# Optimization experiments

Hardware: AMD Instinct MI355X
Metric: run time of the kernel (lower is better)

## Reference

```python
import jax, jax.numpy as jnp
import numpy as np

B, S, D, H = 4, 2048, 1024, 16
HD = D // H  # head_dim = 64

def setup_inputs() -> dict:
    key = jax.random.key(0)
    ks = jax.random.split(key, 5)
    scale = 1.0 / np.sqrt(D)
    return {
        "x": jax.random.normal(ks[0], (B, S, D), dtype=jnp.float32),
        "Wqkv": jax.random.normal(ks[1], (D, 3 * D), dtype=jnp.float32) * scale,
        "bqkv": jax.random.normal(ks[2], (3 * D,), dtype=jnp.float32) * 0.01,
        "Wo": jax.random.normal(ks[3], (D, D), dtype=jnp.float32) * scale,
        "bo": jax.random.normal(ks[4], (D,), dtype=jnp.float32) * 0.01,
    }

def reference(x, Wqkv, bqkv, Wo, bo):
    b, s, d = x.shape
    # fused QKV projection: [B,S,3D]
    qkv = jnp.einsum("bsd,de->bse", x, Wqkv) + bqkv
    # [B,S,H,3*HD] -> [B,H,S,3*HD], then chunk into q,k,v per head
    qkv = qkv.reshape(b, s, H, 3 * HD).transpose(0, 2, 1, 3)
    q, k, v = jnp.split(qkv, 3, axis=-1)  # each [B,H,S,HD]
    inv_sqrt_dk = jnp.asarray(1.0 / np.sqrt(HD), dtype=x.dtype)
    scores = jnp.einsum("bhqd,bhkd->bhqk", q, k) * inv_sqrt_dk
    attn = jax.nn.softmax(scores, axis=-1)
    values = jnp.einsum("bhqk,bhkd->bhqd", attn, v)  # [B,H,S,HD]
    # NOTE: source reshapes [B,H,S,HD] -> [B,S,H*HD] WITHOUT permuting back
    # (a quirk of the original code); replicated faithfully.
    values = values.reshape(b, s, d)
    out = jnp.einsum("bsd,de->bse", values, Wo) + bo
    return out
```

## Files before the change

### kernel.cpp

```cpp
#include <hip/hip_runtime.h>
#include <hip/hip_bf16.h>
#include <cstdint>

static constexpr int Bq  = 4;
static constexpr int Sq  = 2048;
static constexpr int Dq  = 1024;
static constexpr int Hq  = 16;
static constexpr int HDq = 64;
static constexpr int ROWS = Bq * Sq;
static constexpr int QKV_N = 3 * Dq;

typedef __bf16 bf16x8 __attribute__((ext_vector_type(8)));
typedef __bf16 bf16x4 __attribute__((ext_vector_type(4)));
typedef __bf16 bf16x2 __attribute__((ext_vector_type(2)));
typedef float  floatx4 __attribute__((ext_vector_type(4)));
typedef float  floatx16 __attribute__((ext_vector_type(16)));
typedef unsigned int uintx4 __attribute__((ext_vector_type(4)));

#define MFMA16(a, b, c) __builtin_amdgcn_mfma_f32_16x16x32_bf16((a), (b), (c), 0, 0, 0)
#define MFMA32(a, b, c) __builtin_amdgcn_mfma_f32_32x32x16_bf16((a), (b), (c), 0, 0, 0)

#define QSCALE 0.18033688011112042f

__device__ __forceinline__ void async16(const void* g, void* l) {
    __builtin_amdgcn_global_load_lds(
        (const __attribute__((address_space(1))) uint32_t*)g,
        (__attribute__((address_space(3))) uint32_t*)l, 16, 0, 0);
}

__global__ __launch_bounds__(256) void prep_kernel(const float4* __restrict__ x4,
                                                   bf16x4* __restrict__ xb4,
                                                   const float* __restrict__ Wqkv,
                                                   __bf16* __restrict__ WqkvT,
                                                   const float* __restrict__ Wo,
                                                   __bf16* __restrict__ WoT) {
    __shared__ float t[32][33];
    const int bx = blockIdx.x;
    if (bx < 8192) {
        int i = bx * 256 + threadIdx.x;
        float4 v = x4[i];
        bf16x4 o;
        o[0] = (__bf16)v.x; o[1] = (__bf16)v.y; o[2] = (__bf16)v.z; o[3] = (__bf16)v.w;
        xb4[i] = o;
        return;
    }
    const float* in; __bf16* out; int K, N, bid;
    if (bx < 8192 + 3072) { bid = bx - 8192;  in = Wqkv; out = WqkvT; K = Dq; N = QKV_N; }
    else                  { bid = bx - 11264; in = Wo;   out = WoT;   K = Dq; N = Dq; }
    const int nt = N / 32;
    const int n0 = (bid % nt) * 32, k0 = (bid / nt) * 32;
    const int c = threadIdx.x & 31, r0 = threadIdx.x >> 5;
#pragma unroll
    for (int rr = 0; rr < 32; rr += 8)
        t[r0 + rr][c] = in[(size_t)(k0 + r0 + rr) * N + n0 + c];
    __syncthreads();
#pragma unroll
    for (int rr = 0; rr < 32; rr += 8)
        out[(size_t)(n0 + r0 + rr) * K + k0 + c] = (__bf16)t[c][r0 + rr];
}

__global__ __launch_bounds__(512, 2) void gemm_qkv_kernel(const __bf16* __restrict__ A,
                                                          const __bf16* __restrict__ BT,
                                                          const float* __restrict__ bias,
                                                          __bf16* __restrict__ qkvb,
                                                          __bf16* __restrict__ Vt) {
    __shared__ __bf16 lds[2][7][64][64];

    const int tid  = threadIdx.x;
    const int lane = tid & 63;
    const int wave = tid >> 6;
    const int wm = wave >> 1;
    const int wn = wave & 1;
    const int l31 = lane & 31;
    const int hi  = lane >> 5;
    const int kx  = l31 & 7;

    const int m0 = blockIdx.y * 256;
    const int n0 = blockIdx.x * 192;

    const int sw = ((lane & 7) ^ (lane >> 3)) * 8;
    const __bf16* gA = A  + (size_t)(m0 + wave * 8 + (lane >> 3)) * 1024 + sw;
    const __bf16* gB = BT + (size_t)(n0 + wave * 8 + (lane >> 3)) * 1024 + sw;

    auto STAGEA = [&](int buf, int u, int ktel) {
        async16(gA + (size_t)u * 65536 + ktel, &lds[buf][u][0][0] + wave * 512 + lane * 8);
    };
    auto STAGEB = [&](int buf, int j, int ktel) {
        async16(gB + (size_t)j * 65536 + ktel, &lds[buf][4 + j][0][0] + wave * 512 + lane * 8);
    };

    floatx16 acc[2][3] = {};

#pragma unroll
    for (int u = 0; u < 4; ++u) STAGEA(0, u, 0);
#pragma unroll
    for (int j = 0; j < 3; ++j) STAGEB(0, j, 0);
#pragma unroll
    for (int u = 0; u < 4; ++u) STAGEA(1, u, 64);
    asm volatile("s_waitcnt vmcnt(4)" ::: "memory");
    __builtin_amdgcn_sched_barrier(0);
    __builtin_amdgcn_s_barrier();

    bf16x8 af[2][4], bf[4];

    for (int t = 0; t < 16; ++t) {
        const int d = t & 1;

#pragma unroll
        for (int fm = 0; fm < 2; ++fm)
#pragma unroll
            for (int ks = 0; ks < 4; ++ks)
                af[fm][ks] = *(const bf16x8*)(&lds[d][wm][fm * 32 + l31][((ks * 2 + hi) ^ kx) * 8]);
        {
            const int br = wn * 96;
#pragma unroll
            for (int ks = 0; ks < 4; ++ks)
                bf[ks] = *(const bf16x8*)(&lds[d][4 + (br >> 6)][(br & 63) + l31][((ks * 2 + hi) ^ kx) * 8]);
        }
        if (t + 1 < 16) {
            STAGEB(d ^ 1, 0, (t + 1) * 64);
            STAGEB(d ^ 1, 1, (t + 1) * 64);
            STAGEB(d ^ 1, 2, (t + 1) * 64);
        }
        __builtin_amdgcn_s_barrier();
        __builtin_amdgcn_s_setprio(1);
#pragma unroll
        for (int ks = 0; ks < 4; ++ks) {
            acc[0][0] = MFMA32(af[0][ks], bf[ks], acc[0][0]);
            acc[1][0] = MFMA32(af[1][ks], bf[ks], acc[1][0]);
        }
        __builtin_amdgcn_s_setprio(0);
        __builtin_amdgcn_s_barrier();

        {
            const int br = wn * 96 + 32;
#pragma unroll
            for (int ks = 0; ks < 4; ++ks)
                bf[ks] = *(const bf16x8*)(&lds[d][4 + (br >> 6)][(br & 63) + l31][((ks * 2 + hi) ^ kx) * 8]);
        }
        if (t + 2 < 16) {
            STAGEA(d, 0, (t + 2) * 64);
            STAGEA(d, 1, (t + 2) * 64);
        }
        __builtin_amdgcn_s_barrier();
        __builtin_amdgcn_s_setprio(1);
#pragma unroll
        for (int ks = 0; ks < 4; ++ks) {
            acc[0][1] = MFMA32(af[0][ks], bf[ks], acc[0][1]);
            acc[1][1] = MFMA32(af[1][ks], bf[ks], acc[1][1]);
        }
        __builtin_amdgcn_s_setprio(0);
        __builtin_amdgcn_s_barrier();

        {
            const int br = wn * 96 + 64;
#pragma unroll
            for (int ks = 0; ks < 4; ++ks)
                bf[ks] = *(const bf16x8*)(&lds[d][4 + (br >> 6)][(br & 63) + l31][((ks * 2 + hi) ^ kx) * 8]);
        }
        if (t + 2 < 16) {
            STAGEA(d, 2, (t + 2) * 64);
            STAGEA(d, 3, (t + 2) * 64);
        }
        __builtin_amdgcn_s_barrier();
        __builtin_amdgcn_s_setprio(1);
#pragma unroll
        for (int ks = 0; ks < 4; ++ks) {
            acc[0][2] = MFMA32(af[0][ks], bf[ks], acc[0][2]);
            acc[1][2] = MFMA32(af[1][ks], bf[ks], acc[1][2]);
        }
        __builtin_amdgcn_s_setprio(0);
        if (t < 14) {
            asm volatile("s_waitcnt vmcnt(4)" ::: "memory");
        } else {
            asm volatile("s_waitcnt vmcnt(0)" ::: "memory");
        }
        __builtin_amdgcn_sched_barrier(0);
        __builtin_amdgcn_s_barrier();
    }

#pragma unroll
    for (int fn = 0; fn < 3; ++fn) {
        const int cm = wn * 96 + fn * 32;
        const int cg = n0 + cm;
        const float bv = bias[cg + l31];
        if (cm >= 128) {
            const int hh = n0 / 192;
            const int dd = cm - 128 + l31;
            const int bb = m0 >> 11;
            const int sb = (m0 & 2047) + wm * 64;
            __bf16* vt = Vt + ((size_t)(bb * Hq + hh) * HDq + dd) * Sq + sb;
#pragma unroll
            for (int fm = 0; fm < 2; ++fm)
#pragma unroll
                for (int g = 0; g < 4; ++g) {
                    bf16x4 vv;
#pragma unroll
                    for (int i = 0; i < 4; ++i) vv[i] = (__bf16)(acc[fm][fn][g * 4 + i] + bv);
                    *(bf16x4*)(vt + fm * 32 + g * 8 + hi * 4) = vv;
                }
        } else {
            const float sc = (cm < 64) ? QSCALE : 1.0f;
#pragma unroll
            for (int fm = 0; fm < 2; ++fm)
#pragma unroll
                for (int r = 0; r < 16; ++r) {
                    int m = m0 + wm * 64 + fm * 32 + (r & 3) + 8 * (r >> 2) + 4 * hi;
                    qkvb[(size_t)m * QKV_N + cg + l31] = (__bf16)((acc[fm][fn][r] + bv) * sc);
                }
        }
    }
}

__global__ __launch_bounds__(512, 2) void gemm_out_kernel(const __bf16* __restrict__ A,
                                                          const __bf16* __restrict__ BT,
                                                          const float* __restrict__ bias,
                                                          float* __restrict__ Cout) {
    __shared__ __bf16 lds[2][6][64][64];

    const int tid  = threadIdx.x;
    const int lane = tid & 63;
    const int wave = tid >> 6;
    const int wm = wave >> 1;
    const int wn = wave & 1;
    const int l31 = lane & 31;
    const int hi  = lane >> 5;
    const int kx  = l31 & 7;

    const int m0 = blockIdx.y * 256;
    const int n0 = blockIdx.x * 128;

    const int sw = ((lane & 7) ^ (lane >> 3)) * 8;
    const __bf16* gA = A  + (size_t)(m0 + wave * 8 + (lane >> 3)) * 1024 + sw;
    const __bf16* gB = BT + (size_t)(n0 + wave * 8 + (lane >> 3)) * 1024 + sw;

    auto STAGEA = [&](int buf, int u, int ktel) {
        async16(gA + (size_t)u * 65536 + ktel, &lds[buf][u][0][0] + wave * 512 + lane * 8);
    };
    auto STAGEB = [&](int buf, int j, int ktel) {
        async16(gB + (size_t)j * 65536 + ktel, &lds[buf][4 + j][0][0] + wave * 512 + lane * 8);
    };

    floatx16 acc[2][2] = {};

#pragma unroll
    for (int u = 0; u < 4; ++u) STAGEA(0, u, 0);
#pragma unroll
    for (int j = 0; j < 2; ++j) STAGEB(0, j, 0);
#pragma unroll
    for (int u = 0; u < 4; ++u) STAGEA(1, u, 64);
    asm volatile("s_waitcnt vmcnt(4)" ::: "memory");
    __builtin_amdgcn_sched_barrier(0);
    __builtin_amdgcn_s_barrier();

    bf16x8 af[2][4], bf[4];

    for (int t = 0; t < 16; ++t) {
        const int d = t & 1;

#pragma unroll
        for (int fm = 0; fm < 2; ++fm)
#pragma unroll
            for (int ks = 0; ks < 4; ++ks)
                af[fm][ks] = *(const bf16x8*)(&lds[d][wm][fm * 32 + l31][((ks * 2 + hi) ^ kx) * 8]);
#pragma unroll
        for (int ks = 0; ks < 4; ++ks)
            bf[ks] = *(const bf16x8*)(&lds[d][4 + wn][l31][((ks * 2 + hi) ^ kx) * 8]);
        if (t + 1 < 16) {
            STAGEB(d ^ 1, 0, (t + 1) * 64);
            STAGEB(d ^ 1, 1, (t + 1) * 64);
        }
        __builtin_amdgcn_s_barrier();
        __builtin_amdgcn_s_setprio(1);
#pragma unroll
        for (int ks = 0; ks < 4; ++ks) {
            acc[0][0] = MFMA32(af[0][ks], bf[ks], acc[0][0]);
            acc[1][0] = MFMA32(af[1][ks], bf[ks], acc[1][0]);
        }
        __builtin_amdgcn_s_setprio(0);
        __builtin_amdgcn_s_barrier();

#pragma unroll
        for (int ks = 0; ks < 4; ++ks)
            bf[ks] = *(const bf16x8*)(&lds[d][4 + wn][32 + l31][((ks * 2 + hi) ^ kx) * 8]);
        if (t + 2 < 16) {
            STAGEA(d, 0, (t + 2) * 64);
            STAGEA(d, 1, (t + 2) * 64);
            STAGEA(d, 2, (t + 2) * 64);
            STAGEA(d, 3, (t + 2) * 64);
        }
        __builtin_amdgcn_s_barrier();
        __builtin_amdgcn_s_setprio(1);
#pragma unroll
        for (int ks = 0; ks < 4; ++ks) {
            acc[0][1] = MFMA32(af[0][ks], bf[ks], acc[0][1]);
            acc[1][1] = MFMA32(af[1][ks], bf[ks], acc[1][1]);
        }
        __builtin_amdgcn_s_setprio(0);
        if (t < 14) {
            asm volatile("s_waitcnt vmcnt(4)" ::: "memory");
        } else {
            asm volatile("s_waitcnt vmcnt(0)" ::: "memory");
        }
        __builtin_amdgcn_sched_barrier(0);
        __builtin_amdgcn_s_barrier();
    }

#pragma unroll
    for (int fn = 0; fn < 2; ++fn) {
        const int col = n0 + wn * 64 + fn * 32 + l31;
        const float bv = bias[col];
#pragma unroll
        for (int fm = 0; fm < 2; ++fm)
#pragma unroll
            for (int r = 0; r < 16; ++r) {
                int row = m0 + wm * 64 + fm * 32 + (r & 3) + 8 * (r >> 2) + 4 * hi;
                Cout[(size_t)row * Dq + col] = acc[fm][fn][r] + bv;
            }
    }
}

__global__ __launch_bounds__(256, 2) void attn_kernel(const __bf16* __restrict__ qkv,
                                                      const __bf16* __restrict__ Vt,
                                                      __bf16* __restrict__ v2) {
    const int bh = blockIdx.x;
    const int b = bh >> 4, h = bh & 15;
    const int q0 = blockIdx.y * 256;
    const int tid  = threadIdx.x;
    const int lane = tid & 63;
    const int wave = tid >> 6;
    const int l31  = lane & 31;
    const int hi   = lane >> 5;
    const int kx   = l31 & 7;
    const size_t rs = QKV_N;
    const __bf16* base  = qkv + (size_t)b * Sq * rs + (size_t)h * (3 * HDq);
    const __bf16* vbase = Vt + (size_t)bh * HDq * Sq;

    __shared__ alignas(16) __bf16 Ks[2][64][64];
    __shared__ alignas(16) __bf16 Vs[2][64][64];

    bf16x8 qb[2][4];
#pragma unroll
    for (int qg = 0; qg < 2; ++qg) {
        const __bf16* qr = base + (size_t)(q0 + wave * 64 + qg * 32 + l31) * rs + hi * 8;
#pragma unroll
        for (int st = 0; st < 4; ++st) qb[qg][st] = *(const bf16x8*)(qr + st * 16);
    }

    const int rA = wave * 8 + (lane >> 3);
    const int rB = rA + 32;
    const int sw = ((lane & 7) ^ (rA & 7)) * 8;
    const __bf16* gK0 = base + HDq + (size_t)rA * rs + sw;
    const __bf16* gK1 = base + HDq + (size_t)rB * rs + sw;
    const __bf16* gV0 = vbase + (size_t)rA * Sq + sw;
    const __bf16* gV1 = vbase + (size_t)rB * Sq + sw;
    const int loff0 = wave * 512 + lane * 8;
    const int loff1 = (4 + wave) * 512 + lane * 8;

    auto STAGE = [&](int bufi, int kt) {
        const size_t ko = (size_t)kt * rs;
        async16(gK0 + ko, &Ks[bufi][0][0] + loff0);
        async16(gK1 + ko, &Ks[bufi][0][0] + loff1);
        async16(gV0 + kt, &Vs[bufi][0][0] + loff0);
        async16(gV1 + kt, &Vs[bufi][0][0] + loff1);
    };

    auto softmax_pb = [&](const floatx16& c, float& la, bf16x8* pb) {
        unsigned int W[8];
        float s0 = 0.f, s1 = 0.f;
#pragma unroll
        for (int m = 0; m < 8; ++m) {
            float e0 = __builtin_amdgcn_exp2f(c[2 * m]);
            float e1 = __builtin_amdgcn_exp2f(c[2 * m + 1]);
            s0 += e0; s1 += e1;
            union { bf16x2 v; unsigned int u; } pk;
            pk.v[0] = (__bf16)e0; pk.v[1] = (__bf16)e1;
            W[m] = pk.u;
        }
        la += s0 + s1;
#pragma unroll
        for (int ks = 0; ks < 2; ++ks) {
            auto r0 = __builtin_amdgcn_permlane32_swap(W[ks * 4 + 0], W[ks * 4 + 2], false, false);
            auto r1 = __builtin_amdgcn_permlane32_swap(W[ks * 4 + 1], W[ks * 4 + 3], false, false);
            uintx4 bb; bb[0] = r0[0]; bb[1] = r1[0]; bb[2] = r0[1]; bb[3] = r1[1];
            pb[ks] = __builtin_bit_cast(bf16x8, bb);
        }
    };

    floatx16 o[2][2] = {};
    float la0 = 0.f, la1 = 0.f;

    STAGE(0, 0);
    __syncthreads();

    int cur = 0;
    for (int kt = 0; kt < Sq; kt += 64, cur ^= 1) {
        if (kt + 64 < Sq) STAGE(cur ^ 1, kt + 64);

        bf16x8 ka0[4], ka1[4];
#pragma unroll
        for (int st = 0; st < 4; ++st) {
            ka0[st] = *(const bf16x8*)(&Ks[cur][l31][((st * 2 + hi) ^ kx) * 8]);
            ka1[st] = *(const bf16x8*)(&Ks[cur][32 + l31][((st * 2 + hi) ^ kx) * 8]);
        }
        floatx16 c00 = {}, c01 = {}, c10 = {}, c11 = {};
        __builtin_amdgcn_s_setprio(1);
#pragma unroll
        for (int st = 0; st < 4; ++st) {
            c00 = MFMA32(ka0[st], qb[0][st], c00);
            c10 = MFMA32(ka1[st], qb[0][st], c10);
            c01 = MFMA32(ka0[st], qb[1][st], c01);
            c11 = MFMA32(ka1[st], qb[1][st], c11);
        }
        __builtin_amdgcn_s_setprio(0);

        bf16x8 pb00[2], pb01[2], pb10[2], pb11[2];
        softmax_pb(c00, la0, pb00);
        softmax_pb(c01, la1, pb01);
        __builtin_amdgcn_s_setprio(1);
#pragma unroll
        for (int ks = 0; ks < 2; ++ks) {
            const int kslot = ks * 2 + hi;
            bf16x8 va0 = *(const bf16x8*)(&Vs[cur][l31][(kslot ^ kx) * 8]);
            bf16x8 va1 = *(const bf16x8*)(&Vs[cur][32 + l31][(kslot ^ kx) * 8]);
            o[0][0] = MFMA32(va0, pb00[ks], o[0][0]);
            o[0][1] = MFMA32(va1, pb00[ks], o[0][1]);
            o[1][0] = MFMA32(va0, pb01[ks], o[1][0]);
            o[1][1] = MFMA32(va1, pb01[ks], o[1][1]);
        }
        __builtin_amdgcn_s_setprio(0);
        softmax_pb(c10, la0, pb10);
        softmax_pb(c11, la1, pb11);
        __builtin_amdgcn_s_setprio(1);
#pragma unroll
        for (int ks = 0; ks < 2; ++ks) {
            const int kslot = 4 + ks * 2 + hi;
            bf16x8 va0 = *(const bf16x8*)(&Vs[cur][l31][(kslot ^ kx) * 8]);
            bf16x8 va1 = *(const bf16x8*)(&Vs[cur][32 + l31][(kslot ^ kx) * 8]);
            o[0][0] = MFMA32(va0, pb10[ks], o[0][0]);
            o[0][1] = MFMA32(va1, pb10[ks], o[0][1]);
            o[1][0] = MFMA32(va0, pb11[ks], o[1][0]);
            o[1][1] = MFMA32(va1, pb11[ks], o[1][1]);
        }
        __builtin_amdgcn_s_setprio(0);

        __syncthreads();
    }

#pragma unroll
    for (int qg = 0; qg < 2; ++qg) {
        float lsum = qg ? la1 : la0;
        float l = lsum + __shfl_xor(lsum, 32);
        float rinv = 1.0f / l;
        const int q = q0 + wave * 64 + qg * 32 + l31;
        size_t row = (size_t)b * Sq + h * 128 + (q >> 4);
        __bf16* vrow = v2 + row * Dq + (size_t)(q & 15) * 64;
#pragma unroll
        for (int gg = 0; gg < 4; ++gg) {
            bf16x4 ov;
#pragma unroll
            for (int i = 0; i < 4; ++i) ov[i] = (__bf16)(o[qg][0][gg * 4 + i] * rinv);
            *(bf16x4*)(vrow + gg * 8 + hi * 4) = ov;
#pragma unroll
            for (int i = 0; i < 4; ++i) ov[i] = (__bf16)(o[qg][1][gg * 4 + i] * rinv);
            *(bf16x4*)(vrow + 32 + gg * 8 + hi * 4) = ov;
        }
    }
}

extern "C" void kernel_launch(void* const* d_in, const int* in_sizes, int n_in,
                              void* d_out, int out_size, void* d_ws, size_t ws_size,
                              hipStream_t stream) {
    const float* x    = (const float*)d_in[0];
    const float* Wqkv = (const float*)d_in[1];
    const float* bqkv = (const float*)d_in[2];
    const float* Wo   = (const float*)d_in[3];
    const float* bo   = (const float*)d_in[4];
    float* out = (float*)d_out;

    __bf16* xb    = (__bf16*)d_ws;
    __bf16* WqkvT = xb    + (size_t)ROWS * Dq;
    __bf16* WoT   = WqkvT + (size_t)QKV_N * Dq;
    __bf16* qkvb  = WoT   + (size_t)Dq * Dq;
    __bf16* Vt    = qkvb  + (size_t)ROWS * QKV_N;
    __bf16* v2    = xb;

    prep_kernel<<<12288, 256, 0, stream>>>((const float4*)x, (bf16x4*)xb,
                                           Wqkv, WqkvT, Wo, WoT);

    gemm_qkv_kernel<<<dim3(QKV_N / 192, ROWS / 256), 512, 0, stream>>>(
        xb, WqkvT, bqkv, qkvb, Vt);

    attn_kernel<<<dim3(Bq * Hq, Sq / 256), 256, 0, stream>>>(qkvb, Vt, v2);

    gemm_out_kernel<<<dim3(Dq / 128, ROWS / 256), 512, 0, stream>>>(
        v2, WoT, bo, out);
}
```

Measured before the change: 250.8 us.

## Triple-buffer K/V tiles in attention with vmcnt-based waits instead of syncthreads

Grows the K/V shared-memory staging from two buffers to three, so loads run two tiles ahead of compute. The full __syncthreads at the end of each iteration becomes a partial s_waitcnt vmcnt plus a raw s_barrier, so newer prefetches can stay in flight across the barrier. The aim is to hide global-load latency better, at the cost of more LDS per block. The correctness of the vmcnt thresholds depends on how many memory ops async16 issues per call.

After: 250.8 us. About the same (+0.0%).

```diff
diff --git a/kernel.cpp b/kernel.cpp
--- a/kernel.cpp
+++ b/kernel.cpp
@@ -336,8 +336,8 @@
     const __bf16* base  = qkv + (size_t)b * Sq * rs + (size_t)h * (3 * HDq);
     const __bf16* vbase = Vt + (size_t)bh * HDq * Sq;
 
-    __shared__ alignas(16) __bf16 Ks[2][64][64];
-    __shared__ alignas(16) __bf16 Vs[2][64][64];
+    __shared__ alignas(16) __bf16 Ks[3][64][64];
+    __shared__ alignas(16) __bf16 Vs[3][64][64];
 
     bf16x8 qb[2][4];
 #pragma unroll
@@ -359,10 +359,12 @@
 
     auto STAGE = [&](int bufi, int kt) {
         const size_t ko = (size_t)kt * rs;
-        async16(gK0 + ko, &Ks[bufi][0][0] + loff0);
-        async16(gK1 + ko, &Ks[bufi][0][0] + loff1);
-        async16(gV0 + kt, &Vs[bufi][0][0] + loff0);
-        async16(gV1 + kt, &Vs[bufi][0][0] + loff1);
+        __bf16* KsD = &Ks[bufi][0][0];
+        __bf16* VsD = &Vs[bufi][0][0];
+        async16(gK0 + ko, KsD + loff0);
+        async16(gK1 + ko, KsD + loff1);
+        async16(gV0 + kt, VsD + loff0);
+        async16(gV1 + kt, VsD + loff1);
     };
 
     auto softmax_pb = [&](const floatx16& c, float& la, bf16x8* pb) {
@@ -391,11 +393,18 @@
     float la0 = 0.f, la1 = 0.f;
 
     STAGE(0, 0);
-    __syncthreads();
-
+    STAGE(1, 64);
+    asm volatile("s_waitcnt vmcnt(8)" ::: "memory");
+    __builtin_amdgcn_sched_barrier(0);
+    __builtin_amdgcn_s_barrier();
+
+    constexpr int NT = Sq / 64;
     int cur = 0;
-    for (int kt = 0; kt < Sq; kt += 64, cur ^= 1) {
-        if (kt + 64 < Sq) STAGE(cur ^ 1, kt + 64);
+    for (int t = 0; t < NT; ++t) {
+        if (t + 2 < NT) {
+            int nb = cur + 2; if (nb >= 3) nb -= 3;
+            STAGE(nb, (t + 2) * 64);
+        }
 
         bf16x8 ka0[4], ka1[4];
 #pragma unroll
@@ -444,7 +453,16 @@
         }
         __builtin_amdgcn_s_setprio(0);
 
-        __syncthreads();
+        if (t + 1 < NT) {
+            if (t + 2 < NT) {
+                asm volatile("s_waitcnt vmcnt(8)" ::: "memory");
+            } else {
+                asm volatile("s_waitcnt vmcnt(0)" ::: "memory");
+            }
+            __builtin_amdgcn_sched_barrier(0);
+            __builtin_amdgcn_s_barrier();
+        }
+        if (++cur >= 3) cur = 0;
     }
 
 #pragma unroll
```
